# Kernel optimization log

Hardware: AMD Instinct MI355X
Metric: run time of the kernel (lower is better)

## Reference

```python
import jax, jax.numpy as jnp
import numpy as np

B, N, C = 4, 4096, 256
NUM_HEADS = 8
NUM_GROUPS = 4  # num_groups2, recursive_index=True path
HEAD_DIM = C // NUM_HEADS
SCALE = HEAD_DIM ** -0.5


def setup_inputs() -> dict:
    key = jax.random.key(0)
    k_x, k_idx, k_qkv, k_proj, k_pb = jax.random.split(key, 5)
    x = jax.random.normal(k_x, (B, N, C), dtype=jnp.float32)
    idx = jax.random.permutation(k_idx, N)  # random token shuffle (torch.randperm)
    # nn.Linear params (torch convention: y = x @ W.T + b)
    w_qkv = jax.random.normal(k_qkv, (3 * C, C), dtype=jnp.float32) * (1.0 / np.sqrt(C))
    w_proj = jax.random.normal(k_proj, (C, C), dtype=jnp.float32) * (1.0 / np.sqrt(C))
    b_proj = jax.random.normal(k_pb, (C,), dtype=jnp.float32) * 0.01
    return {"x": x, "idx": idx, "w_qkv": w_qkv, "w_proj": w_proj, "b_proj": b_proj}


def reference(x, idx, w_qkv, w_proj, b_proj):
    g, H, d = NUM_GROUPS, NUM_HEADS, HEAD_DIM
    n = N // g  # tokens per group
    inverse = jnp.argsort(idx)
    xp = x[:, idx, :]  # shuffled tokens [B, N, C]
    # qkv projection then split into groups/heads: [B, g, n, 3, H, d]
    qkv = (xp @ w_qkv.T).reshape(B, g, n, 3, H, d)
    q = qkv[:, :, :, 0].transpose(0, 1, 3, 2, 4)  # [B, g, H, n, d]
    k = qkv[:, :, :, 1].transpose(0, 1, 3, 2, 4)
    v = qkv[:, :, :, 2].transpose(0, 1, 3, 2, 4)
    attn = jnp.einsum('bghnd,bghmd->bghnm', q, k) * SCALE  # [B, g, H, n, n]
    attn = jax.nn.softmax(attn, axis=-1)
    o = jnp.einsum('bghnm,bghmd->bghnd', attn, v)
    # [B, g, H, n, d] -> [B, g, n, H, d] -> [B, N, C] (group-major token order)
    o = o.transpose(0, 1, 3, 2, 4).reshape(B, N, C)
    o = o[:, inverse, :]  # undo the shuffle
    return o @ w_proj.T + b_proj
```

## Files before the change

### kernel.cpp

```cpp
#include <hip/hip_runtime.h>
#include <hip/hip_bf16.h>


typedef __attribute__((ext_vector_type(8))) short bf16x8;
typedef __attribute__((ext_vector_type(4))) float f32x4;

__device__ __forceinline__ unsigned short f2bf(float x){
  __hip_bfloat16 h = __float2bfloat16(x);
  return __builtin_bit_cast(unsigned short, h);
}

__device__ __forceinline__ bf16x8 cvt8(const float4 f0, const float4 f1){
  bf16x8 v;
  v[0]=(short)f2bf(f0.x); v[1]=(short)f2bf(f0.y);
  v[2]=(short)f2bf(f0.z); v[3]=(short)f2bf(f0.w);
  v[4]=(short)f2bf(f1.x); v[5]=(short)f2bf(f1.y);
  v[6]=(short)f2bf(f1.z); v[7]=(short)f2bf(f1.w);
  return v;
}

#define QSCALE (0.17677669529663687f * 1.4426950408889634f)


__global__ __launch_bounds__(256, 3) void qkv_gemm(
    const float* __restrict__ x, const int* __restrict__ idx,
    const float* __restrict__ w_qkv,
    unsigned short* __restrict__ Qb, unsigned short* __restrict__ KF,
    unsigned short* __restrict__ VF)
{
  __shared__ __align__(16) unsigned short Asl[128*64];
  __shared__ __align__(16) unsigned short Bsl[128*64];
  const int tid = threadIdx.x;
  const int bx = blockIdx.x, by = blockIdx.y;
  const int m0 = bx << 7;
  const int bb = bx >> 5;
  const int gg = (bx >> 3) & 3;
  const int j0 = (bx & 31) << 7;
  const int n0 = by << 7;

  int srow[2], brow[2], wb[2];
  #pragma unroll
  for (int it = 0; it < 2; ++it){
    int c = (it << 8) + tid;
    int row = c >> 2;
    int k8 = (c & 3) << 3;
    srow[it] = (bb << 12) + idx[j0 + row];
    brow[it] = n0 + row;
    wb[it] = ((row << 7) + (k8 << 1)) ^ ((row & 7) << 4);
  }

  #pragma unroll
  for (int it = 0; it < 2; ++it){
    int k8 = (((it << 8) + tid) & 3) << 3;
    const float* xs = x + srow[it]*256 + k8;
    const float* wsp = w_qkv + brow[it]*256 + k8;
    *(bf16x8*)((char*)Asl + wb[it]) = cvt8(*(const float4*)(xs), *(const float4*)(xs+4));
    *(bf16x8*)((char*)Bsl + wb[it]) = cvt8(*(const float4*)(wsp), *(const float4*)(wsp+4));
  }
  __syncthreads();

  const int lane = tid & 63;
  const int w = tid >> 6, wr = w >> 1, wc = w & 1;
  const int lr = lane & 15, lg = lane >> 4;
  const int ka = lg << 3;

  f32x4 acc[4][4];
  #pragma unroll
  for (int il = 0; il < 4; ++il)
    #pragma unroll
    for (int jl = 0; jl < 4; ++jl)
      acc[il][jl] = (f32x4){0.f,0.f,0.f,0.f};

  for (int st = 0; st < 8; ++st){
    float4 a0[2], a1[2], c0[2], c1[2];
    const bool pf = (st < 7);
    if (pf){
      int kb = (st + 1) << 5;
      #pragma unroll
      for (int it = 0; it < 2; ++it){
        int k8 = (((it << 8) + tid) & 3) << 3;
        const float* xs = x + srow[it]*256 + kb + k8;
        const float* wsp = w_qkv + brow[it]*256 + kb + k8;
        a0[it] = *(const float4*)(xs);  a1[it] = *(const float4*)(xs + 4);
        c0[it] = *(const float4*)(wsp); c1[it] = *(const float4*)(wsp + 4);
      }
    }

    bf16x8 af[4], bfr[4];
    #pragma unroll
    for (int il = 0; il < 4; ++il){
      int rowA = (wr << 6) + (il << 4) + lr;
      af[il] = *(const bf16x8*)((const char*)Asl + (((rowA << 7) + (ka << 1)) ^ ((rowA & 7) << 4)));
      int rowB = (wc << 6) + (il << 4) + lr;
      bfr[il] = *(const bf16x8*)((const char*)Bsl + (((rowB << 7) + (ka << 1)) ^ ((rowB & 7) << 4)));
    }
    __builtin_amdgcn_s_setprio(1);
    #pragma unroll
    for (int il = 0; il < 4; ++il)
      #pragma unroll
      for (int jl = 0; jl < 4; ++jl)
        acc[il][jl] = __builtin_amdgcn_mfma_f32_16x16x32_bf16(af[il], bfr[jl], acc[il][jl], 0, 0, 0);
    __builtin_amdgcn_s_setprio(0);

    __syncthreads();
    if (pf){
      #pragma unroll
      for (int it = 0; it < 2; ++it){
        *(bf16x8*)((char*)Asl + wb[it]) = cvt8(a0[it], a1[it]);
        *(bf16x8*)((char*)Bsl + wb[it]) = cvt8(c0[it], c1[it]);
      }
      __syncthreads();
    }
  }

  const int s = by >> 1;
  const int hbase = ((bb << 2) + gg) << 3;
  #pragma unroll
  for (int il = 0; il < 4; ++il){
    int mr0 = m0 + (wr << 6) + (il << 4) + (lg << 2);
    int nl0 = mr0 & 1023;
    int t   = nl0 >> 5;
    #pragma unroll
    for (int jl = 0; jl < 4; ++jl){
      int ocol = ((by & 1) << 7) + (wc << 6) + (jl << 4) + lr;
      int h  = ocol >> 5, dd = ocol & 31;
      int head = hbase + h;
      if (s == 2){
        int m = nl0 & 31;
        int lane2 = ((m >> 3) << 4) + (dd & 15);
        int half = dd >> 4;
        ushort4 pk;
        pk.x = f2bf(acc[il][jl][0]); pk.y = f2bf(acc[il][jl][1]);
        pk.z = f2bf(acc[il][jl][2]); pk.w = f2bf(acc[il][jl][3]);
        *(ushort4*)(VF + head*32768 + t*1024 + half*512 + lane2*8 + (m & 7)) = pk;
      } else if (s == 1){
        int r0 = nl0 & 31;
        int f  = (r0 >> 2) & 1;
        unsigned short* dst = KF + head*32768 + t*1024 + f*512
                             + ((((dd >> 3) << 4) + ((r0 >> 3) << 2)) << 3) + (dd & 7);
        dst[0]  = f2bf(acc[il][jl][0]);
        dst[8]  = f2bf(acc[il][jl][1]);
        dst[16] = f2bf(acc[il][jl][2]);
        dst[24] = f2bf(acc[il][jl][3]);
      } else {
        unsigned short* dst = Qb + head*32768 + dd;
        #pragma unroll
        for (int q = 0; q < 4; ++q)
          dst[(nl0 + q) << 5] = f2bf(acc[il][jl][q] * QSCALE);
      }
    }
  }
}

__device__ __forceinline__ void softmax16(
    const f32x4 s0, const f32x4 s1, const f32x4 s2, const f32x4 s3,
    bf16x8& pf0, bf16x8& pf1)
{
  float p0=__builtin_amdgcn_exp2f(s0[0]);  float p1=__builtin_amdgcn_exp2f(s0[1]);
  float p2=__builtin_amdgcn_exp2f(s0[2]);  float p3=__builtin_amdgcn_exp2f(s0[3]);
  float p4=__builtin_amdgcn_exp2f(s1[0]);  float p5=__builtin_amdgcn_exp2f(s1[1]);
  float p6=__builtin_amdgcn_exp2f(s1[2]);  float p7=__builtin_amdgcn_exp2f(s1[3]);
  float p8=__builtin_amdgcn_exp2f(s2[0]);  float p9=__builtin_amdgcn_exp2f(s2[1]);
  float p10=__builtin_amdgcn_exp2f(s2[2]); float p11=__builtin_amdgcn_exp2f(s2[3]);
  float p12=__builtin_amdgcn_exp2f(s3[0]); float p13=__builtin_amdgcn_exp2f(s3[1]);
  float p14=__builtin_amdgcn_exp2f(s3[2]); float p15=__builtin_amdgcn_exp2f(s3[3]);

  pf0[0]=(short)f2bf(p0);  pf0[1]=(short)f2bf(p1);
  pf0[2]=(short)f2bf(p2);  pf0[3]=(short)f2bf(p3);
  pf0[4]=(short)f2bf(p4);  pf0[5]=(short)f2bf(p5);
  pf0[6]=(short)f2bf(p6);  pf0[7]=(short)f2bf(p7);
  pf1[0]=(short)f2bf(p8);  pf1[1]=(short)f2bf(p9);
  pf1[2]=(short)f2bf(p10); pf1[3]=(short)f2bf(p11);
  pf1[4]=(short)f2bf(p12); pf1[5]=(short)f2bf(p13);
  pf1[6]=(short)f2bf(p14); pf1[7]=(short)f2bf(p15);
}

__global__ __launch_bounds__(256, 4) void attn_kernel(
    const unsigned short* __restrict__ Qb, const unsigned short* __restrict__ KF,
    const unsigned short* __restrict__ VF, unsigned short* __restrict__ OB)
{
  __shared__ __align__(16) char lds[32768];
  const int tid  = threadIdx.x;
  const int head = blockIdx.x >> 3;
  const int qblk = blockIdx.x & 7;
  const int lane = tid & 63;
  const int w  = tid >> 6;
  const int lr = lane & 15, lg = lane >> 4;
  const int q0 = qblk * 128 + w * 32;

  const unsigned short* kf = KF + head*32768;
  const unsigned short* vf = VF + head*32768;
  const unsigned short* qbase = Qb + head*32768;

  {
    bf16x8 k0 = *(const bf16x8*)(kf + tid*8);
    bf16x8 k1 = *(const bf16x8*)(kf + 2048 + tid*8);
    bf16x8 v0 = *(const bf16x8*)(vf + tid*8);
    bf16x8 v1 = *(const bf16x8*)(vf + 2048 + tid*8);
    *(bf16x8*)(lds + tid*16)          = k0;
    *(bf16x8*)(lds + 4096 + tid*16)   = k1;
    *(bf16x8*)(lds + 8192 + tid*16)   = v0;
    *(bf16x8*)(lds + 12288 + tid*16)  = v1;
  }
  bf16x8 qfA = *(const bf16x8*)(qbase + (q0 + lr)*32 + (lg << 3));
  bf16x8 qfB = *(const bf16x8*)(qbase + (q0 + 16 + lr)*32 + (lg << 3));

  const short one_bf = (short)0x3F80;
  bf16x8 onesf = {one_bf,one_bf,one_bf,one_bf,one_bf,one_bf,one_bf,one_bf};

  f32x4 o0A={0.f,0.f,0.f,0.f}, o1A={0.f,0.f,0.f,0.f};
  f32x4 o0B={0.f,0.f,0.f,0.f}, o1B={0.f,0.f,0.f,0.f};
  f32x4 lsA={0.f,0.f,0.f,0.f}, lsB={0.f,0.f,0.f,0.f};
  const f32x4 zz={0.f,0.f,0.f,0.f};

  __syncthreads();
  int cur = 0;
  for (int it = 0; it < 8; ++it){
    bf16x8 kr0, kr1, vr0, vr1;
    const bool pf = (it < 7);
    if (pf){
      const unsigned short* kg = kf + (it+1)*4096 + tid*8;
      const unsigned short* vg = vf + (it+1)*4096 + tid*8;
      kr0 = *(const bf16x8*)(kg);
      kr1 = *(const bf16x8*)(kg + 2048);
      vr0 = *(const bf16x8*)(vg);
      vr1 = *(const bf16x8*)(vg + 2048);
    }

    const char* KL = lds + cur*16384 + lane*16;
    const char* VL = KL + 8192;
    #pragma unroll
    for (int hh = 0; hh < 2; ++hh){
      const char* kp_ = KL + hh*4096;
      const char* vp_ = VL + hh*4096;
      bf16x8 kA0 = *(const bf16x8*)(kp_);
      bf16x8 kB0 = *(const bf16x8*)(kp_ + 1024);
      bf16x8 kA1 = *(const bf16x8*)(kp_ + 2048);
      bf16x8 kB1 = *(const bf16x8*)(kp_ + 3072);
      bf16x8 v00 = *(const bf16x8*)(vp_);
      bf16x8 v01 = *(const bf16x8*)(vp_ + 1024);
      bf16x8 v10 = *(const bf16x8*)(vp_ + 2048);
      bf16x8 v11 = *(const bf16x8*)(vp_ + 3072);

      __builtin_amdgcn_s_setprio(1);
      f32x4 sA0A = __builtin_amdgcn_mfma_f32_16x16x32_bf16(kA0, qfA, zz, 0, 0, 0);
      f32x4 sB0A = __builtin_amdgcn_mfma_f32_16x16x32_bf16(kB0, qfA, zz, 0, 0, 0);
      f32x4 sA1A = __builtin_amdgcn_mfma_f32_16x16x32_bf16(kA1, qfA, zz, 0, 0, 0);
      f32x4 sB1A = __builtin_amdgcn_mfma_f32_16x16x32_bf16(kB1, qfA, zz, 0, 0, 0);
      f32x4 sA0B = __builtin_amdgcn_mfma_f32_16x16x32_bf16(kA0, qfB, zz, 0, 0, 0);
      f32x4 sB0B = __builtin_amdgcn_mfma_f32_16x16x32_bf16(kB0, qfB, zz, 0, 0, 0);
      f32x4 sA1B = __builtin_amdgcn_mfma_f32_16x16x32_bf16(kA1, qfB, zz, 0, 0, 0);
      f32x4 sB1B = __builtin_amdgcn_mfma_f32_16x16x32_bf16(kB1, qfB, zz, 0, 0, 0);
      __builtin_amdgcn_s_setprio(0);

      bf16x8 pf0A, pf1A, pf0B, pf1B;
      softmax16(sA0A, sB0A, sA1A, sB1A, pf0A, pf1A);
      __builtin_amdgcn_s_setprio(1);
      o0A = __builtin_amdgcn_mfma_f32_16x16x32_bf16(pf0A, v00, o0A, 0, 0, 0);
      o1A = __builtin_amdgcn_mfma_f32_16x16x32_bf16(pf0A, v01, o1A, 0, 0, 0);
      o0A = __builtin_amdgcn_mfma_f32_16x16x32_bf16(pf1A, v10, o0A, 0, 0, 0);
      o1A = __builtin_amdgcn_mfma_f32_16x16x32_bf16(pf1A, v11, o1A, 0, 0, 0);
      lsA = __builtin_amdgcn_mfma_f32_16x16x32_bf16(pf0A, onesf, lsA, 0, 0, 0);
      lsA = __builtin_amdgcn_mfma_f32_16x16x32_bf16(pf1A, onesf, lsA, 0, 0, 0);
      __builtin_amdgcn_s_setprio(0);
      softmax16(sA0B, sB0B, sA1B, sB1B, pf0B, pf1B);
      __builtin_amdgcn_s_setprio(1);
      o0B = __builtin_amdgcn_mfma_f32_16x16x32_bf16(pf0B, v00, o0B, 0, 0, 0);
      o1B = __builtin_amdgcn_mfma_f32_16x16x32_bf16(pf0B, v01, o1B, 0, 0, 0);
      o0B = __builtin_amdgcn_mfma_f32_16x16x32_bf16(pf1B, v10, o0B, 0, 0, 0);
      o1B = __builtin_amdgcn_mfma_f32_16x16x32_bf16(pf1B, v11, o1B, 0, 0, 0);
      lsB = __builtin_amdgcn_mfma_f32_16x16x32_bf16(pf0B, onesf, lsB, 0, 0, 0);
      lsB = __builtin_amdgcn_mfma_f32_16x16x32_bf16(pf1B, onesf, lsB, 0, 0, 0);
      __builtin_amdgcn_s_setprio(0);
    }

    if (pf){
      char* db = lds + (cur^1)*16384;
      *(bf16x8*)(db + tid*16)          = kr0;
      *(bf16x8*)(db + 4096 + tid*16)   = kr1;
      *(bf16x8*)(db + 8192 + tid*16)   = vr0;
      *(bf16x8*)(db + 12288 + tid*16)  = vr1;
    }
    __syncthreads();
    cur ^= 1;
  }

  const int bI = head >> 5, gI = (head >> 3) & 3, hI = head & 7;
  unsigned short* obase = OB + (bI*4096 + gI*1024 + q0)*256 + hI*32;
  #pragma unroll
  for (int q = 0; q < 4; ++q){
    float iA = 1.0f / lsA[q];
    obase[((lg << 2) + q)*256 + lr]      = f2bf(o0A[q] * iA);
    obase[((lg << 2) + q)*256 + 16 + lr] = f2bf(o1A[q] * iA);
    float iB = 1.0f / lsB[q];
    obase[(16 + (lg << 2) + q)*256 + lr]      = f2bf(o0B[q] * iB);
    obase[(16 + (lg << 2) + q)*256 + 16 + lr] = f2bf(o1B[q] * iB);
  }
}

__global__ __launch_bounds__(256) void proj_gemm(
    const unsigned short* __restrict__ OB, const float* __restrict__ w_proj,
    const float* __restrict__ b_proj, const int* __restrict__ idx,
    float* __restrict__ out)
{
  __shared__ unsigned short Alds[64*256];
  __shared__ unsigned short Blds[64*256];
  const int tid = threadIdx.x;
  const int m0 = blockIdx.x << 6;
  const int bb = m0 >> 12;

  #pragma unroll
  for (int it = 0; it < 8; ++it){
    int c = (it << 8) + tid;
    int row = c >> 5;
    int k8 = (c & 31) << 3;
    int byt = ((row << 9) + (k8 << 1)) ^ ((row & 7) << 4);
    *(bf16x8*)((char*)Alds + byt) = *(const bf16x8*)(OB + (m0+row)*256 + k8);
  }

  const int w  = tid >> 6, lane = tid & 63;
  const int lr = lane & 15, lg = lane >> 4;
  const int wr = w >> 1,  wc = w & 1;

  for (int nt = 0; nt < 2; ++nt){
    const int n0 = blockIdx.y * 128 + nt * 64;
    __syncthreads();
    #pragma unroll
    for (int it = 0; it < 8; ++it){
      int c = (it << 8) + tid;
      int row = c >> 5;
      int k8 = (c & 31) << 3;
      const float4 f0 = *(const float4*)(w_proj + (n0+row)*256 + k8);
      const float4 f1 = *(const float4*)(w_proj + (n0+row)*256 + k8 + 4);
      bf16x8 v;
      v[0]=(short)f2bf(f0.x); v[1]=(short)f2bf(f0.y);
      v[2]=(short)f2bf(f0.z); v[3]=(short)f2bf(f0.w);
      v[4]=(short)f2bf(f1.x); v[5]=(short)f2bf(f1.y);
      v[6]=(short)f2bf(f1.z); v[7]=(short)f2bf(f1.w);
      int byt = ((row << 9) + (k8 << 1)) ^ ((row & 7) << 4);
      *(bf16x8*)((char*)Blds + byt) = v;
    }
    __syncthreads();

    f32x4 acc[2][2];
    #pragma unroll
    for (int i=0;i<2;++i)
      #pragma unroll
      for (int j=0;j<2;++j)
        acc[i][j] = (f32x4){0.f,0.f,0.f,0.f};

    #pragma unroll
    for (int ks = 0; ks < 8; ++ks){
      bf16x8 af[2], bfr[2];
      int ka = (ks << 5) + (lg << 3);
      #pragma unroll
      for (int i=0;i<2;++i){
        int rowA = (wr << 5) + (i << 4) + lr;
        int bytA = ((rowA << 9) + (ka << 1)) ^ ((rowA & 7) << 4);
        af[i] = *(const bf16x8*)((const char*)Alds + bytA);
        int rowB = (wc << 5) + (i << 4) + lr;
        int bytB = ((rowB << 9) + (ka << 1)) ^ ((rowB & 7) << 4);
        bfr[i] = *(const bf16x8*)((const char*)Blds + bytB);
      }
      #pragma unroll
      for (int i=0;i<2;++i)
        #pragma unroll
        for (int j=0;j<2;++j)
          acc[i][j] = __builtin_amdgcn_mfma_f32_16x16x32_bf16(af[i], bfr[j], acc[i][j], 0, 0, 0);
    }

    #pragma unroll
    for (int i=0;i<2;++i){
      int mr0 = m0 + (wr << 5) + (i << 4) + (lg << 2);
      int rd[4];
      #pragma unroll
      for (int q=0;q<4;++q)
        rd[q] = (bb << 12) + idx[(mr0 + q) & 4095];
      #pragma unroll
      for (int j=0;j<2;++j){
        int o = n0 + (wc << 5) + (j << 4) + lr;
        float bias = b_proj[o];
        #pragma unroll
        for (int q=0;q<4;++q)
          out[rd[q]*256 + o] = acc[i][j][q] + bias;
      }
    }
  }
}

extern "C" void kernel_launch(void* const* d_in, const int* in_sizes, int n_in,
                              void* d_out, int out_size, void* d_ws, size_t ws_size,
                              hipStream_t stream)
{
  const float* x      = (const float*)d_in[0];
  const int*   idx    = (const int*)  d_in[1];
  const float* w_qkv  = (const float*)d_in[2];
  const float* w_proj = (const float*)d_in[3];
  const float* b_proj = (const float*)d_in[4];
  float* out = (float*)d_out;

  char* ws = (char*)d_ws;
  unsigned short* Qb = (unsigned short*)(ws);
  unsigned short* KF = (unsigned short*)(ws + (8u  << 20));
  unsigned short* VF = (unsigned short*)(ws + (16u << 20));
  unsigned short* OB = (unsigned short*)(ws + (24u << 20));

  qkv_gemm<<<dim3(128, 6), 256, 0, stream>>>(x, idx, w_qkv, Qb, KF, VF);
  attn_kernel<<<dim3(1024), 256, 0, stream>>>(Qb, KF, VF, OB);
  proj_gemm<<<dim3(256, 2), 256, 0, stream>>>(OB, w_proj, b_proj, idx, out);
}
```

Measured before the change: 60.99 us.

## Process 64 query rows per wave in attention with software-pipelined QK MFMAs

Each wave of the attention kernel now handles 64 query rows (four 16-row groups) instead of 32, which halves the grid to 512 blocks and halves how often K/V are loaded into LDS and staged per query. Inside the loop, the QK score MFMAs for the next group are issued before the softmax of the current group, so matrix work overlaps the exp/convert ALU work. The cost is more accumulator and Q registers per thread, reflected in the occupancy hint dropping to 2, and fewer blocks to spread across CUs.

New measurement: 57.88 us. 1.05x faster.

```diff
diff --git a/kernel.cpp b/kernel.cpp
--- a/kernel.cpp
+++ b/kernel.cpp
@@ -175,18 +175,18 @@
   pf1[6]=(short)f2bf(p14); pf1[7]=(short)f2bf(p15);
 }
 
-__global__ __launch_bounds__(256, 4) void attn_kernel(
+__global__ __launch_bounds__(256, 2) void attn_kernel(
     const unsigned short* __restrict__ Qb, const unsigned short* __restrict__ KF,
     const unsigned short* __restrict__ VF, unsigned short* __restrict__ OB)
 {
   __shared__ __align__(16) char lds[32768];
   const int tid  = threadIdx.x;
-  const int head = blockIdx.x >> 3;
-  const int qblk = blockIdx.x & 7;
+  const int head = blockIdx.x >> 2;
+  const int qblk = blockIdx.x & 3;
   const int lane = tid & 63;
   const int w  = tid >> 6;
   const int lr = lane & 15, lg = lane >> 4;
-  const int q0 = qblk * 128 + w * 32;
+  const int q0 = qblk * 256 + w * 64;
 
   const unsigned short* kf = KF + head*32768;
   const unsigned short* vf = VF + head*32768;
@@ -202,23 +202,30 @@
     *(bf16x8*)(lds + 8192 + tid*16)   = v0;
     *(bf16x8*)(lds + 12288 + tid*16)  = v1;
   }
-  bf16x8 qfA = *(const bf16x8*)(qbase + (q0 + lr)*32 + (lg << 3));
-  bf16x8 qfB = *(const bf16x8*)(qbase + (q0 + 16 + lr)*32 + (lg << 3));
+
+  bf16x8 qf[4];
+  #pragma unroll
+  for (int g = 0; g < 4; ++g)
+    qf[g] = *(const bf16x8*)(qbase + (q0 + g*16 + lr)*32 + (lg << 3));
 
   const short one_bf = (short)0x3F80;
   bf16x8 onesf = {one_bf,one_bf,one_bf,one_bf,one_bf,one_bf,one_bf,one_bf};
 
-  f32x4 o0A={0.f,0.f,0.f,0.f}, o1A={0.f,0.f,0.f,0.f};
-  f32x4 o0B={0.f,0.f,0.f,0.f}, o1B={0.f,0.f,0.f,0.f};
-  f32x4 lsA={0.f,0.f,0.f,0.f}, lsB={0.f,0.f,0.f,0.f};
+  f32x4 o0[4], o1[4], ls[4];
+  #pragma unroll
+  for (int g = 0; g < 4; ++g){
+    o0[g] = (f32x4){0.f,0.f,0.f,0.f};
+    o1[g] = (f32x4){0.f,0.f,0.f,0.f};
+    ls[g] = (f32x4){0.f,0.f,0.f,0.f};
+  }
   const f32x4 zz={0.f,0.f,0.f,0.f};
 
   __syncthreads();
   int cur = 0;
   for (int it = 0; it < 8; ++it){
     bf16x8 kr0, kr1, vr0, vr1;
-    const bool pf = (it < 7);
-    if (pf){
+    const bool pfch = (it < 7);
+    if (pfch){
       const unsigned short* kg = kf + (it+1)*4096 + tid*8;
       const unsigned short* vg = vf + (it+1)*4096 + tid*8;
       kr0 = *(const bf16x8*)(kg);
@@ -243,38 +250,38 @@
       bf16x8 v11 = *(const bf16x8*)(vp_ + 3072);
 
       __builtin_amdgcn_s_setprio(1);
-      f32x4 sA0A = __builtin_amdgcn_mfma_f32_16x16x32_bf16(kA0, qfA, zz, 0, 0, 0);
-      f32x4 sB0A = __builtin_amdgcn_mfma_f32_16x16x32_bf16(kB0, qfA, zz, 0, 0, 0);
-      f32x4 sA1A = __builtin_amdgcn_mfma_f32_16x16x32_bf16(kA1, qfA, zz, 0, 0, 0);
-      f32x4 sB1A = __builtin_amdgcn_mfma_f32_16x16x32_bf16(kB1, qfA, zz, 0, 0, 0);
-      f32x4 sA0B = __builtin_amdgcn_mfma_f32_16x16x32_bf16(kA0, qfB, zz, 0, 0, 0);
-      f32x4 sB0B = __builtin_amdgcn_mfma_f32_16x16x32_bf16(kB0, qfB, zz, 0, 0, 0);
-      f32x4 sA1B = __builtin_amdgcn_mfma_f32_16x16x32_bf16(kA1, qfB, zz, 0, 0, 0);
-      f32x4 sB1B = __builtin_amdgcn_mfma_f32_16x16x32_bf16(kB1, qfB, zz, 0, 0, 0);
+      f32x4 sA0 = __builtin_amdgcn_mfma_f32_16x16x32_bf16(kA0, qf[0], zz, 0, 0, 0);
+      f32x4 sB0 = __builtin_amdgcn_mfma_f32_16x16x32_bf16(kB0, qf[0], zz, 0, 0, 0);
+      f32x4 sA1 = __builtin_amdgcn_mfma_f32_16x16x32_bf16(kA1, qf[0], zz, 0, 0, 0);
+      f32x4 sB1 = __builtin_amdgcn_mfma_f32_16x16x32_bf16(kB1, qf[0], zz, 0, 0, 0);
       __builtin_amdgcn_s_setprio(0);
 
-      bf16x8 pf0A, pf1A, pf0B, pf1B;
-      softmax16(sA0A, sB0A, sA1A, sB1A, pf0A, pf1A);
-      __builtin_amdgcn_s_setprio(1);
-      o0A = __builtin_amdgcn_mfma_f32_16x16x32_bf16(pf0A, v00, o0A, 0, 0, 0);
-      o1A = __builtin_amdgcn_mfma_f32_16x16x32_bf16(pf0A, v01, o1A, 0, 0, 0);
-      o0A = __builtin_amdgcn_mfma_f32_16x16x32_bf16(pf1A, v10, o0A, 0, 0, 0);
-      o1A = __builtin_amdgcn_mfma_f32_16x16x32_bf16(pf1A, v11, o1A, 0, 0, 0);
-      lsA = __builtin_amdgcn_mfma_f32_16x16x32_bf16(pf0A, onesf, lsA, 0, 0, 0);
-      lsA = __builtin_amdgcn_mfma_f32_16x16x32_bf16(pf1A, onesf, lsA, 0, 0, 0);
-      __builtin_amdgcn_s_setprio(0);
-      softmax16(sA0B, sB0B, sA1B, sB1B, pf0B, pf1B);
-      __builtin_amdgcn_s_setprio(1);
-      o0B = __builtin_amdgcn_mfma_f32_16x16x32_bf16(pf0B, v00, o0B, 0, 0, 0);
-      o1B = __builtin_amdgcn_mfma_f32_16x16x32_bf16(pf0B, v01, o1B, 0, 0, 0);
-      o0B = __builtin_amdgcn_mfma_f32_16x16x32_bf16(pf1B, v10, o0B, 0, 0, 0);
-      o1B = __builtin_amdgcn_mfma_f32_16x16x32_bf16(pf1B, v11, o1B, 0, 0, 0);
-      lsB = __builtin_amdgcn_mfma_f32_16x16x32_bf16(pf0B, onesf, lsB, 0, 0, 0);
-      lsB = __builtin_amdgcn_mfma_f32_16x16x32_bf16(pf1B, onesf, lsB, 0, 0, 0);
-      __builtin_amdgcn_s_setprio(0);
-    }
-
-    if (pf){
+      #pragma unroll
+      for (int g = 0; g < 4; ++g){
+        f32x4 nA0, nB0, nA1, nB1;
+        if (g < 3){
+          __builtin_amdgcn_s_setprio(1);
+          nA0 = __builtin_amdgcn_mfma_f32_16x16x32_bf16(kA0, qf[g+1], zz, 0, 0, 0);
+          nB0 = __builtin_amdgcn_mfma_f32_16x16x32_bf16(kB0, qf[g+1], zz, 0, 0, 0);
+          nA1 = __builtin_amdgcn_mfma_f32_16x16x32_bf16(kA1, qf[g+1], zz, 0, 0, 0);
+          nB1 = __builtin_amdgcn_mfma_f32_16x16x32_bf16(kB1, qf[g+1], zz, 0, 0, 0);
+          __builtin_amdgcn_s_setprio(0);
+        }
+        bf16x8 pf0, pf1;
+        softmax16(sA0, sB0, sA1, sB1, pf0, pf1);
+        __builtin_amdgcn_s_setprio(1);
+        o0[g] = __builtin_amdgcn_mfma_f32_16x16x32_bf16(pf0, v00, o0[g], 0, 0, 0);
+        o1[g] = __builtin_amdgcn_mfma_f32_16x16x32_bf16(pf0, v01, o1[g], 0, 0, 0);
+        o0[g] = __builtin_amdgcn_mfma_f32_16x16x32_bf16(pf1, v10, o0[g], 0, 0, 0);
+        o1[g] = __builtin_amdgcn_mfma_f32_16x16x32_bf16(pf1, v11, o1[g], 0, 0, 0);
+        ls[g] = __builtin_amdgcn_mfma_f32_16x16x32_bf16(pf0, onesf, ls[g], 0, 0, 0);
+        ls[g] = __builtin_amdgcn_mfma_f32_16x16x32_bf16(pf1, onesf, ls[g], 0, 0, 0);
+        __builtin_amdgcn_s_setprio(0);
+        if (g < 3){ sA0 = nA0; sB0 = nB0; sA1 = nA1; sB1 = nB1; }
+      }
+    }
+
+    if (pfch){
       char* db = lds + (cur^1)*16384;
       *(bf16x8*)(db + tid*16)          = kr0;
       *(bf16x8*)(db + 4096 + tid*16)   = kr1;
@@ -288,13 +295,14 @@
   const int bI = head >> 5, gI = (head >> 3) & 3, hI = head & 7;
   unsigned short* obase = OB + (bI*4096 + gI*1024 + q0)*256 + hI*32;
   #pragma unroll
-  for (int q = 0; q < 4; ++q){
-    float iA = 1.0f / lsA[q];
-    obase[((lg << 2) + q)*256 + lr]      = f2bf(o0A[q] * iA);
-    obase[((lg << 2) + q)*256 + 16 + lr] = f2bf(o1A[q] * iA);
-    float iB = 1.0f / lsB[q];
-    obase[(16 + (lg << 2) + q)*256 + lr]      = f2bf(o0B[q] * iB);
-    obase[(16 + (lg << 2) + q)*256 + 16 + lr] = f2bf(o1B[q] * iB);
+  for (int g = 0; g < 4; ++g){
+    #pragma unroll
+    for (int q = 0; q < 4; ++q){
+      float iv = 1.0f / ls[g][q];
+      int r = (g << 4) + (lg << 2) + q;
+      obase[r*256 + lr]      = f2bf(o0[g][q] * iv);
+      obase[r*256 + 16 + lr] = f2bf(o1[g][q] * iv);
+    }
   }
 }
 
@@ -406,6 +414,6 @@
   unsigned short* OB = (unsigned short*)(ws + (24u << 20));
 
   qkv_gemm<<<dim3(128, 6), 256, 0, stream>>>(x, idx, w_qkv, Qb, KF, VF);
-  attn_kernel<<<dim3(1024), 256, 0, stream>>>(Qb, KF, VF, OB);
+  attn_kernel<<<dim3(512), 256, 0, stream>>>(Qb, KF, VF, OB);
   proj_gemm<<<dim3(256, 2), 256, 0, stream>>>(OB, w_proj, b_proj, idx, out);
 }
```
